# Optimization experiments

Measured on AMD Instinct MI355X. Metric: run time of the kernel, lower is better.

The kernel has to match this reference:

```python
import jax, jax.numpy as jnp
import numpy as np

D_K = 128
NEG_MAX = float(np.finfo(np.float32).max)  # original uses -finfo(float32).max


def setup_inputs() -> dict:
    key = jax.random.key(0)
    kq, kk, kv, km = jax.random.split(key, 4)
    B, S, D = 16, 2048, D_K
    q = jax.random.normal(kq, (B, S, D), dtype=jnp.float32)
    k = jax.random.normal(kk, (B, S, D), dtype=jnp.float32)
    v = jax.random.normal(kv, (B, S, D), dtype=jnp.float32)
    mask = jax.random.randint(km, (B, S, S), 0, 2).astype(jnp.bool_)
    return {"q": q, "k": k, "v": v, "mask": mask}


def reference(q, k, v, mask):
    # scores: [B, S, S] = q @ k^T / sqrt(d_k)
    scale = 1.0 / np.sqrt(D_K).astype(np.float32)
    scores = jnp.einsum('bqd,bkd->bqk', q, k) * scale
    scores = jnp.where(mask, -NEG_MAX, scores)  # masked_fill with -float32 max
    attn = jax.nn.softmax(scores, axis=2)
    return jnp.einsum('bqk,bkd->bqd', attn, v)
```

## Files before the change

### kernel.cpp

```cpp
#include <hip/hip_runtime.h>

#define NTHREADS 256

typedef __attribute__((ext_vector_type(8))) short bf16x8;
typedef __attribute__((ext_vector_type(4))) float f32x4;
typedef __attribute__((ext_vector_type(2))) unsigned uint2v;
typedef __attribute__((ext_vector_type(4))) unsigned uint4v;

constexpr int kB = 16, kS = 2048, kD = 128;
constexpr int QBLK = 64, KBLK = 32;
constexpr int MSTRIDE = 36;
constexpr float kNegMax = -3.402823466e38f;
constexpr float kMClamp = -1e30f;

__device__ __forceinline__ unsigned cvt_pk(float lo, float hi) {
    unsigned r;
    asm("v_cvt_pk_bf16_f32 %0, %1, %2" : "=v"(r) : "v"(lo), "v"(hi));
    return r;
}

#define SWZ(bytecol, row) ((bytecol) ^ (((row) & 7) << 4))
#define SWZV2(bytecol, row) ((bytecol) ^ ((((row) >> 2) & 3) << 4))
#define SWZP2(bytecol, row) ((bytecol) ^ (((row) & 3) << 4))

template<int SPLIT>
__global__ __launch_bounds__(NTHREADS, 4)
void attn_fwd(const float* __restrict__ q, const float* __restrict__ k,
              const float* __restrict__ v, const int* __restrict__ mask,
              float* __restrict__ out, float* __restrict__ ws)
{
    __shared__ __align__(16) char smem[22784];
    char* K_lds  = smem;
    char* VT_lds = smem + 8192;
    char* P_lds  = smem + 16384;
    unsigned char* M_lds = (unsigned char*)(smem + 20480);

    const int tid = threadIdx.x, lane = tid & 63, w = tid >> 6;
    const int l15 = lane & 15, lg = lane >> 4;

    const int bid = (int)blockIdx.x;
    int b, qbase, kbase;
    if (SPLIT == 1) {
        int swz = (bid & 7) * 64 + (bid >> 3);
        b = swz >> 5; qbase = (swz & 31) * QBLK; kbase = 0;
    } else {
        int swz = (bid & 7) * 128 + (bid >> 3);
        b = swz >> 6;
        int rem = swz & 63;
        qbase = (rem >> 1) * QBLK;
        kbase = (rem & 1) * (kS / 2);
    }
    const int nrounds = (SPLIT == 1) ? (kS / KBLK) : (kS / KBLK / 2);

    const float scale = 0.08838834764831845f;
    bf16x8 qf[4];
    {
        const float* qp = q + ((size_t)(b*kS + qbase + w*16 + l15)) * kD;
        #pragma unroll
        for (int kk = 0; kk < 4; ++kk) {
            float4 a = *(const float4*)(qp + kk*32 + lg*8);
            float4 c = *(const float4*)(qp + kk*32 + lg*8 + 4);
            uint4v pk = { cvt_pk(a.x*scale, a.y*scale), cvt_pk(a.z*scale, a.w*scale),
                          cvt_pk(c.x*scale, c.y*scale), cvt_pk(c.z*scale, c.w*scale) };
            qf[kk] = __builtin_bit_cast(bf16x8, pk);
        }
    }

    f32x4 acc[8];
    #pragma unroll
    for (int d = 0; d < 8; ++d) acc[d] = f32x4{0.f,0.f,0.f,0.f};
    float m_r = kMClamp, l_r = 0.f;

    const float* kbat = k + (size_t)b * kS * kD;
    const float* vbat = v + (size_t)b * kS * kD;
    const int*   mbat = mask + ((size_t)b * kS + qbase) * kS;

    char* Pw = P_lds + w * 1024;
    const int kg = tid >> 5, dg = tid & 31;

    float4 kreg[2][2];
    float4 vreg[4];
    int4   mreg[2];

    auto LOAD = [&](int kt0) {
        #pragma unroll
        for (int c = 0; c < 2; ++c) {
            int chunk = c * 256 + tid;
            int row = chunk >> 4, col8 = chunk & 15;
            const float4* ptr = (const float4*)(kbat + (size_t)(kt0 + row)*kD + col8*8);
            kreg[c][0] = ptr[0];
            kreg[c][1] = ptr[1];
        }
        #pragma unroll
        for (int r = 0; r < 4; ++r)
            vreg[r] = *(const float4*)(vbat + (size_t)(kt0 + kg*4 + r)*kD + dg*4);
        #pragma unroll
        for (int c = 0; c < 2; ++c) {
            int idx = c * 256 + tid;
            int mrow = idx >> 3, mc4 = idx & 7;
            mreg[c] = *(const int4*)(mbat + (size_t)mrow*kS + kt0 + mc4*4);
        }
    };

    auto STORE = [&]() {
        #pragma unroll
        for (int c = 0; c < 2; ++c) {
            int chunk = c * 256 + tid;
            int row = chunk >> 4, col8 = chunk & 15;
            uint4v pk = { cvt_pk(kreg[c][0].x, kreg[c][0].y), cvt_pk(kreg[c][0].z, kreg[c][0].w),
                          cvt_pk(kreg[c][1].x, kreg[c][1].y), cvt_pk(kreg[c][1].z, kreg[c][1].w) };
            *(uint4v*)(K_lds + row*256 + SWZ(col8*16, row)) = pk;
        }
        #pragma unroll
        for (int jj = 0; jj < 4; ++jj) {
            int row = dg * 4 + jj;
            uint2v pk = { cvt_pk((&vreg[0].x)[jj], (&vreg[1].x)[jj]),
                          cvt_pk((&vreg[2].x)[jj], (&vreg[3].x)[jj]) };
            *(uint2v*)(VT_lds + row*64 + SWZV2(kg*8, row)) = pk;
        }
        #pragma unroll
        for (int c = 0; c < 2; ++c) {
            int idx = c * 256 + tid;
            int mrow = idx >> 3, mc4 = idx & 7;
            unsigned pk = (unsigned)(mreg[c].x != 0)
                        | ((unsigned)(mreg[c].y != 0) << 8)
                        | ((unsigned)(mreg[c].z != 0) << 16)
                        | ((unsigned)(mreg[c].w != 0) << 24);
            *(unsigned*)(M_lds + mrow*MSTRIDE + mc4*4) = pk;
        }
    };

    LOAD(kbase);

    for (int t = 0; t < nrounds; ++t) {
        __syncthreads();
        STORE();
        __syncthreads();
        if (t + 1 < nrounds) LOAD(kbase + (t + 1) * KBLK);

        f32x4 z[2];
        #pragma unroll
        for (int kt = 0; kt < 2; ++kt) {
            f32x4 zz = f32x4{0.f,0.f,0.f,0.f};
            int krow = kt*16 + l15;
            #pragma unroll
            for (int kk = 0; kk < 4; ++kk) {
                bf16x8 kf = *(const bf16x8*)(K_lds + krow*256 + SWZ(kk*64 + lg*16, krow));
                zz = __builtin_amdgcn_mfma_f32_16x16x32_bf16(kf, qf[kk], zz, 0, 0, 0);
            }
            z[kt] = zz;
        }

        const int mrowb = (w*16 + l15) * MSTRIDE;
        float mx = kNegMax;
        #pragma unroll
        for (int kt = 0; kt < 2; ++kt) {
            unsigned nib = *(const unsigned*)(M_lds + mrowb + kt*16 + lg*4);
            #pragma unroll
            for (int i = 0; i < 4; ++i) {
                float sv = ((nib >> (8*i)) & 0xFFu) ? kNegMax : z[kt][i];
                z[kt][i] = sv;
                mx = fmaxf(mx, sv);
            }
        }
        mx = fmaxf(mx, __shfl_xor(mx, 16));
        mx = fmaxf(mx, __shfl_xor(mx, 32));
        float mnew = fmaxf(m_r, mx);
        float corr = __expf(m_r - mnew);
        float rs = 0.f;
        #pragma unroll
        for (int kt = 0; kt < 2; ++kt) {
            float p0 = __expf(z[kt][0] - mnew);
            float p1 = __expf(z[kt][1] - mnew);
            float p2 = __expf(z[kt][2] - mnew);
            float p3 = __expf(z[kt][3] - mnew);
            rs += (p0 + p1) + (p2 + p3);
            uint2v pk = { cvt_pk(p0, p1), cvt_pk(p2, p3) };
            *(uint2v*)(Pw + l15*64 + SWZP2(kt*32 + lg*8, l15)) = pk;
        }
        rs += __shfl_xor(rs, 16);
        rs += __shfl_xor(rs, 32);
        m_r = mnew;
        l_r = l_r * corr + rs;
        #pragma unroll
        for (int d = 0; d < 8; ++d) acc[d] *= corr;

        bf16x8 pf = *(const bf16x8*)(Pw + l15*64 + SWZP2(lg*16, l15));
        #pragma unroll
        for (int dblk = 0; dblk < 8; ++dblk) {
            int vrow = dblk*16 + l15;
            bf16x8 vf = *(const bf16x8*)(VT_lds + vrow*64 + SWZV2(lg*16, vrow));
            acc[dblk] = __builtin_amdgcn_mfma_f32_16x16x32_bf16(vf, pf, acc[dblk], 0, 0, 0);
        }
    }

    if (SPLIT == 1) {
        float inv = 1.0f / l_r;
        float* op = out + ((size_t)(b*kS + qbase + w*16 + l15)) * kD;
        #pragma unroll
        for (int dblk = 0; dblk < 8; ++dblk) {
            float4 r;
            r.x = acc[dblk][0] * inv;
            r.y = acc[dblk][1] * inv;
            r.z = acc[dblk][2] * inv;
            r.w = acc[dblk][3] * inv;
            *(float4*)(op + dblk*16 + lg*4) = r;
        }
    } else {
        const int half = (kbase != 0);
        const size_t row = (size_t)half * (kB*kS) + (size_t)b*kS + qbase + w*16 + l15;
        float* op = ws + row * kD;
        #pragma unroll
        for (int dblk = 0; dblk < 8; ++dblk) {
            float4 r;
            r.x = acc[dblk][0]; r.y = acc[dblk][1];
            r.z = acc[dblk][2]; r.w = acc[dblk][3];
            *(float4*)(op + dblk*16 + lg*4) = r;
        }
        if (lg == 0) {
            float* ml = ws + (size_t)2*kB*kS*kD;
            ml[row*2 + 0] = m_r;
            ml[row*2 + 1] = l_r;
        }
    }
}

__global__ __launch_bounds__(NTHREADS)
void attn_merge(const float* __restrict__ ws, float* __restrict__ out)
{
    const float* ml = ws + (size_t)2*kB*kS*kD;
    const int tid = threadIdx.x;
    const size_t r = (size_t)blockIdx.x * 8 + (tid >> 5);
    const int c = (tid & 31) * 4;
    float m0 = ml[r*2 + 0],               l0 = ml[r*2 + 1];
    float m1 = ml[((size_t)kB*kS + r)*2], l1 = ml[((size_t)kB*kS + r)*2 + 1];
    float mS = fmaxf(m0, m1);
    float e0 = __expf(m0 - mS), e1 = __expf(m1 - mS);
    float inv = 1.0f / (l0*e0 + l1*e1);
    float4 o0 = *(const float4*)(ws + r*kD + c);
    float4 o1 = *(const float4*)(ws + (size_t)kB*kS*kD + r*kD + c);
    float4 rr;
    rr.x = (o0.x*e0 + o1.x*e1) * inv;
    rr.y = (o0.y*e0 + o1.y*e1) * inv;
    rr.z = (o0.z*e0 + o1.z*e1) * inv;
    rr.w = (o0.w*e0 + o1.w*e1) * inv;
    *(float4*)(out + r*kD + c) = rr;
}

extern "C" void kernel_launch(void* const* d_in, const int* in_sizes, int n_in,
                              void* d_out, int out_size, void* d_ws, size_t ws_size,
                              hipStream_t stream) {
    const float* q = (const float*)d_in[0];
    const float* k = (const float*)d_in[1];
    const float* v = (const float*)d_in[2];
    const int* mask = (const int*)d_in[3];
    float* out = (float*)d_out;
    const size_t wsNeeded = (size_t)2*kB*kS*kD*4 + (size_t)2*kB*kS*2*4;
    if (ws_size >= wsNeeded) {
        attn_fwd<2><<<dim3(kB * (kS/QBLK) * 2), dim3(NTHREADS), 0, stream>>>(
            q, k, v, mask, out, (float*)d_ws);
        attn_merge<<<dim3(kB*kS/8), dim3(NTHREADS), 0, stream>>>((const float*)d_ws, out);
    } else {
        attn_fwd<1><<<dim3(kB * (kS/QBLK)), dim3(NTHREADS), 0, stream>>>(
            q, k, v, mask, out, nullptr);
    }
}
```

Baseline: 126.8 us.

## Double query rows per wave and defer softmax rescaling below threshold

Each wave now processes two 16-row query slices (QBLK 128), so each K and V fragment read from LDS feeds two MFMAs. This halves K/V global traffic and conversion work per query row. The V-transpose and P LDS layouts and their swizzles are reworked to match. The online-softmax rescale of the accumulator is skipped unless the running max grows by more than a threshold, which cuts exp and multiply work. The trade-offs are higher register use, an occupancy hint lowered from 4 to 2, and half as many blocks, which may reduce parallelism on the device.

New measurement: 106.8 us. -15.8%, faster.

```diff
diff --git a/kernel.cpp b/kernel.cpp
--- a/kernel.cpp
+++ b/kernel.cpp
@@ -8,10 +8,11 @@
 typedef __attribute__((ext_vector_type(4))) unsigned uint4v;
 
 constexpr int kB = 16, kS = 2048, kD = 128;
-constexpr int QBLK = 64, KBLK = 32;
+constexpr int QBLK = 128, KBLK = 32;
 constexpr int MSTRIDE = 36;
 constexpr float kNegMax = -3.402823466e38f;
 constexpr float kMClamp = -1e30f;
+constexpr float kDeferThr = 8.0f;
 
 __device__ __forceinline__ unsigned cvt_pk(float lo, float hi) {
     unsigned r;
@@ -20,20 +21,19 @@
 }
 
 #define SWZ(bytecol, row) ((bytecol) ^ (((row) & 7) << 4))
-#define SWZV2(bytecol, row) ((bytecol) ^ ((((row) >> 2) & 3) << 4))
-#define SWZP2(bytecol, row) ((bytecol) ^ (((row) & 3) << 4))
+#define KEYV(d) ((((d) & 7) ^ (((d) >> 2) & 7)) & 7)
 
 template<int SPLIT>
-__global__ __launch_bounds__(NTHREADS, 4)
+__global__ __launch_bounds__(NTHREADS, 2)
 void attn_fwd(const float* __restrict__ q, const float* __restrict__ k,
               const float* __restrict__ v, const int* __restrict__ mask,
               float* __restrict__ out, float* __restrict__ ws)
 {
-    __shared__ __align__(16) char smem[22784];
+    __shared__ __align__(16) char smem[29184];
     char* K_lds  = smem;
     char* VT_lds = smem + 8192;
     char* P_lds  = smem + 16384;
-    unsigned char* M_lds = (unsigned char*)(smem + 20480);
+    unsigned char* M_lds = (unsigned char*)(smem + 24576);
 
     const int tid = threadIdx.x, lane = tid & 63, w = tid >> 6;
     const int l15 = lane & 15, lg = lane >> 4;
@@ -41,46 +41,50 @@
     const int bid = (int)blockIdx.x;
     int b, qbase, kbase;
     if (SPLIT == 1) {
+        int swz = (bid & 7) * 32 + (bid >> 3);
+        b = swz >> 4; qbase = (swz & 15) * QBLK; kbase = 0;
+    } else {
         int swz = (bid & 7) * 64 + (bid >> 3);
-        b = swz >> 5; qbase = (swz & 31) * QBLK; kbase = 0;
-    } else {
-        int swz = (bid & 7) * 128 + (bid >> 3);
-        b = swz >> 6;
-        int rem = swz & 63;
+        b = swz >> 5;
+        int rem = swz & 31;
         qbase = (rem >> 1) * QBLK;
         kbase = (rem & 1) * (kS / 2);
     }
     const int nrounds = (SPLIT == 1) ? (kS / KBLK) : (kS / KBLK / 2);
 
     const float scale = 0.08838834764831845f;
-    bf16x8 qf[4];
-    {
-        const float* qp = q + ((size_t)(b*kS + qbase + w*16 + l15)) * kD;
+    bf16x8 qf[2][4];
+    #pragma unroll
+    for (int qs = 0; qs < 2; ++qs) {
+        const float* qp = q + ((size_t)(b*kS + qbase + w*32 + qs*16 + l15)) * kD;
         #pragma unroll
         for (int kk = 0; kk < 4; ++kk) {
             float4 a = *(const float4*)(qp + kk*32 + lg*8);
             float4 c = *(const float4*)(qp + kk*32 + lg*8 + 4);
             uint4v pk = { cvt_pk(a.x*scale, a.y*scale), cvt_pk(a.z*scale, a.w*scale),
                           cvt_pk(c.x*scale, c.y*scale), cvt_pk(c.z*scale, c.w*scale) };
-            qf[kk] = __builtin_bit_cast(bf16x8, pk);
-        }
-    }
-
-    f32x4 acc[8];
+            qf[qs][kk] = __builtin_bit_cast(bf16x8, pk);
+        }
+    }
+
+    f32x4 acc[2][8];
     #pragma unroll
-    for (int d = 0; d < 8; ++d) acc[d] = f32x4{0.f,0.f,0.f,0.f};
-    float m_r = kMClamp, l_r = 0.f;
+    for (int qs = 0; qs < 2; ++qs)
+        #pragma unroll
+        for (int d = 0; d < 8; ++d) acc[qs][d] = f32x4{0.f,0.f,0.f,0.f};
+    float m_r[2] = {kMClamp, kMClamp};
+    float l_r[2] = {0.f, 0.f};
 
     const float* kbat = k + (size_t)b * kS * kD;
     const float* vbat = v + (size_t)b * kS * kD;
     const int*   mbat = mask + ((size_t)b * kS + qbase) * kS;
 
-    char* Pw = P_lds + w * 1024;
+    char* Pw = P_lds + w * 2048;
     const int kg = tid >> 5, dg = tid & 31;
 
     float4 kreg[2][2];
     float4 vreg[4];
-    int4   mreg[2];
+    int4   mreg[4];
 
     auto LOAD = [&](int kt0) {
         #pragma unroll
@@ -95,7 +99,7 @@
         for (int r = 0; r < 4; ++r)
             vreg[r] = *(const float4*)(vbat + (size_t)(kt0 + kg*4 + r)*kD + dg*4);
         #pragma unroll
-        for (int c = 0; c < 2; ++c) {
+        for (int c = 0; c < 4; ++c) {
             int idx = c * 256 + tid;
             int mrow = idx >> 3, mc4 = idx & 7;
             mreg[c] = *(const int4*)(mbat + (size_t)mrow*kS + kt0 + mc4*4);
@@ -113,13 +117,14 @@
         }
         #pragma unroll
         for (int jj = 0; jj < 4; ++jj) {
-            int row = dg * 4 + jj;
+            int d = dg * 4 + jj;
+            int col = (d >> 6) * 64 + kg * 8;
             uint2v pk = { cvt_pk((&vreg[0].x)[jj], (&vreg[1].x)[jj]),
                           cvt_pk((&vreg[2].x)[jj], (&vreg[3].x)[jj]) };
-            *(uint2v*)(VT_lds + row*64 + SWZV2(kg*8, row)) = pk;
-        }
-        #pragma unroll
-        for (int c = 0; c < 2; ++c) {
+            *(uint2v*)(VT_lds + (d & 63)*128 + (col ^ (KEYV(d) << 4))) = pk;
+        }
+        #pragma unroll
+        for (int c = 0; c < 4; ++c) {
             int idx = c * 256 + tid;
             int mrow = idx >> 3, mc4 = idx & 7;
             unsigned pk = (unsigned)(mreg[c].x != 0)
@@ -138,89 +143,116 @@
         __syncthreads();
         if (t + 1 < nrounds) LOAD(kbase + (t + 1) * KBLK);
 
-        f32x4 z[2];
+        f32x4 z[2][2];
+        #pragma unroll
+        for (int qs = 0; qs < 2; ++qs)
+            #pragma unroll
+            for (int kt = 0; kt < 2; ++kt) z[qs][kt] = f32x4{0.f,0.f,0.f,0.f};
         #pragma unroll
         for (int kt = 0; kt < 2; ++kt) {
-            f32x4 zz = f32x4{0.f,0.f,0.f,0.f};
+            bf16x8 kf[4];
             int krow = kt*16 + l15;
             #pragma unroll
-            for (int kk = 0; kk < 4; ++kk) {
-                bf16x8 kf = *(const bf16x8*)(K_lds + krow*256 + SWZ(kk*64 + lg*16, krow));
-                zz = __builtin_amdgcn_mfma_f32_16x16x32_bf16(kf, qf[kk], zz, 0, 0, 0);
-            }
-            z[kt] = zz;
-        }
-
-        const int mrowb = (w*16 + l15) * MSTRIDE;
-        float mx = kNegMax;
-        #pragma unroll
-        for (int kt = 0; kt < 2; ++kt) {
-            unsigned nib = *(const unsigned*)(M_lds + mrowb + kt*16 + lg*4);
-            #pragma unroll
-            for (int i = 0; i < 4; ++i) {
-                float sv = ((nib >> (8*i)) & 0xFFu) ? kNegMax : z[kt][i];
-                z[kt][i] = sv;
-                mx = fmaxf(mx, sv);
-            }
-        }
-        mx = fmaxf(mx, __shfl_xor(mx, 16));
-        mx = fmaxf(mx, __shfl_xor(mx, 32));
-        float mnew = fmaxf(m_r, mx);
-        float corr = __expf(m_r - mnew);
-        float rs = 0.f;
-        #pragma unroll
-        for (int kt = 0; kt < 2; ++kt) {
-            float p0 = __expf(z[kt][0] - mnew);
-            float p1 = __expf(z[kt][1] - mnew);
-            float p2 = __expf(z[kt][2] - mnew);
-            float p3 = __expf(z[kt][3] - mnew);
-            rs += (p0 + p1) + (p2 + p3);
-            uint2v pk = { cvt_pk(p0, p1), cvt_pk(p2, p3) };
-            *(uint2v*)(Pw + l15*64 + SWZP2(kt*32 + lg*8, l15)) = pk;
-        }
-        rs += __shfl_xor(rs, 16);
-        rs += __shfl_xor(rs, 32);
-        m_r = mnew;
-        l_r = l_r * corr + rs;
-        #pragma unroll
-        for (int d = 0; d < 8; ++d) acc[d] *= corr;
-
-        bf16x8 pf = *(const bf16x8*)(Pw + l15*64 + SWZP2(lg*16, l15));
+            for (int kk = 0; kk < 4; ++kk)
+                kf[kk] = *(const bf16x8*)(K_lds + krow*256 + SWZ(kk*64 + lg*16, krow));
+            #pragma unroll
+            for (int qs = 0; qs < 2; ++qs)
+                #pragma unroll
+                for (int kk = 0; kk < 4; ++kk)
+                    z[qs][kt] = __builtin_amdgcn_mfma_f32_16x16x32_bf16(kf[kk], qf[qs][kk], z[qs][kt], 0, 0, 0);
+        }
+
+        #pragma unroll
+        for (int qs = 0; qs < 2; ++qs) {
+            const int mrowb = (w*32 + qs*16 + l15) * MSTRIDE;
+            float mx = kNegMax;
+            #pragma unroll
+            for (int kt = 0; kt < 2; ++kt) {
+                unsigned nib = *(const unsigned*)(M_lds + mrowb + kt*16 + lg*4);
+                #pragma unroll
+                for (int i = 0; i < 4; ++i) {
+                    float sv = ((nib >> (8*i)) & 0xFFu) ? kNegMax : z[qs][kt][i];
+                    z[qs][kt][i] = sv;
+                    mx = fmaxf(mx, sv);
+                }
+            }
+            mx = fmaxf(mx, __shfl_xor(mx, 16));
+            mx = fmaxf(mx, __shfl_xor(mx, 32));
+            if (!__all(mx <= m_r[qs] + kDeferThr)) {
+                float mnew = fmaxf(m_r[qs], mx);
+                float corr = __expf(m_r[qs] - mnew);
+                l_r[qs] *= corr;
+                #pragma unroll
+                for (int d = 0; d < 8; ++d) acc[qs][d] *= corr;
+                m_r[qs] = mnew;
+            }
+            float rs = 0.f;
+            #pragma unroll
+            for (int kt = 0; kt < 2; ++kt) {
+                float p0 = __expf(z[qs][kt][0] - m_r[qs]);
+                float p1 = __expf(z[qs][kt][1] - m_r[qs]);
+                float p2 = __expf(z[qs][kt][2] - m_r[qs]);
+                float p3 = __expf(z[qs][kt][3] - m_r[qs]);
+                rs += (p0 + p1) + (p2 + p3);
+                uint2v pk = { cvt_pk(p0, p1), cvt_pk(p2, p3) };
+                int col = qs*64 + kt*32 + lg*8;
+                *(uint2v*)(Pw + l15*128 + (col ^ ((l15 & 7) << 4))) = pk;
+            }
+            rs += __shfl_xor(rs, 16);
+            rs += __shfl_xor(rs, 32);
+            l_r[qs] += rs;
+        }
+
+        bf16x8 pf[2];
+        #pragma unroll
+        for (int qs = 0; qs < 2; ++qs) {
+            int col = qs*64 + lg*16;
+            pf[qs] = *(const bf16x8*)(Pw + l15*128 + (col ^ ((l15 & 7) << 4)));
+        }
         #pragma unroll
         for (int dblk = 0; dblk < 8; ++dblk) {
-            int vrow = dblk*16 + l15;
-            bf16x8 vf = *(const bf16x8*)(VT_lds + vrow*64 + SWZV2(lg*16, vrow));
-            acc[dblk] = __builtin_amdgcn_mfma_f32_16x16x32_bf16(vf, pf, acc[dblk], 0, 0, 0);
+            int d = dblk*16 + l15;
+            int col = (d >> 6) * 64 + lg*16;
+            bf16x8 vf = *(const bf16x8*)(VT_lds + (d & 63)*128 + (col ^ (KEYV(d) << 4)));
+            #pragma unroll
+            for (int qs = 0; qs < 2; ++qs)
+                acc[qs][dblk] = __builtin_amdgcn_mfma_f32_16x16x32_bf16(vf, pf[qs], acc[qs][dblk], 0, 0, 0);
         }
     }
 
     if (SPLIT == 1) {
-        float inv = 1.0f / l_r;
-        float* op = out + ((size_t)(b*kS + qbase + w*16 + l15)) * kD;
-        #pragma unroll
-        for (int dblk = 0; dblk < 8; ++dblk) {
-            float4 r;
-            r.x = acc[dblk][0] * inv;
-            r.y = acc[dblk][1] * inv;
-            r.z = acc[dblk][2] * inv;
-            r.w = acc[dblk][3] * inv;
-            *(float4*)(op + dblk*16 + lg*4) = r;
+        #pragma unroll
+        for (int qs = 0; qs < 2; ++qs) {
+            float inv = 1.0f / l_r[qs];
+            float* op = out + ((size_t)(b*kS + qbase + w*32 + qs*16 + l15)) * kD;
+            #pragma unroll
+            for (int dblk = 0; dblk < 8; ++dblk) {
+                float4 r;
+                r.x = acc[qs][dblk][0] * inv;
+                r.y = acc[qs][dblk][1] * inv;
+                r.z = acc[qs][dblk][2] * inv;
+                r.w = acc[qs][dblk][3] * inv;
+                *(float4*)(op + dblk*16 + lg*4) = r;
+            }
         }
     } else {
         const int half = (kbase != 0);
-        const size_t row = (size_t)half * (kB*kS) + (size_t)b*kS + qbase + w*16 + l15;
-        float* op = ws + row * kD;
-        #pragma unroll
-        for (int dblk = 0; dblk < 8; ++dblk) {
-            float4 r;
-            r.x = acc[dblk][0]; r.y = acc[dblk][1];
-            r.z = acc[dblk][2]; r.w = acc[dblk][3];
-            *(float4*)(op + dblk*16 + lg*4) = r;
-        }
-        if (lg == 0) {
-            float* ml = ws + (size_t)2*kB*kS*kD;
-            ml[row*2 + 0] = m_r;
-            ml[row*2 + 1] = l_r;
+        #pragma unroll
+        for (int qs = 0; qs < 2; ++qs) {
+            const size_t row = (size_t)half * (kB*kS) + (size_t)b*kS + qbase + w*32 + qs*16 + l15;
+            float* op = ws + row * kD;
+            #pragma unroll
+            for (int dblk = 0; dblk < 8; ++dblk) {
+                float4 r;
+                r.x = acc[qs][dblk][0]; r.y = acc[qs][dblk][1];
+                r.z = acc[qs][dblk][2]; r.w = acc[qs][dblk][3];
+                *(float4*)(op + dblk*16 + lg*4) = r;
+            }
+            if (lg == 0) {
+                float* ml = ws + (size_t)2*kB*kS*kD;
+                ml[row*2 + 0] = m_r[qs];
+                ml[row*2 + 1] = l_r[qs];
+            }
         }
     }
 }
```
